# Kernel tuning notes

Measured on AMD Instinct MI355X. Metric: run time of the kernel, lower is better.

The kernel has to match this reference:

```python
import jax, jax.numpy as jnp
import numpy as np

B, S, HID = 2, 2048, 1024
H, D = 16, 64
R = 128  # max_relative_position
NREL = 2 * R + 1


def _make_indices():
    i = np.arange(S)[:, None]
    j = np.arange(S)[None, :]
    return np.clip(j - i + R, 0, 2 * R).astype(np.int32)  # [S, S]


def setup_inputs() -> dict:
    key = jax.random.key(0)
    ks = jax.random.split(key, 10)
    sc = 0.02
    return {
        "hidden_states": jax.random.normal(ks[0], (B, S, HID), jnp.float32),
        "st_mask": jnp.ones((B, S), jnp.float32),
        "Wq": jax.random.normal(ks[1], (HID, HID), jnp.float32) * sc,
        "bq": jnp.zeros((HID,), jnp.float32),
        "Wk": jax.random.normal(ks[2], (HID, HID), jnp.float32) * sc,
        "bk": jnp.zeros((HID,), jnp.float32),
        "Wv": jax.random.normal(ks[3], (HID, HID), jnp.float32) * sc,
        "bv": jnp.zeros((HID,), jnp.float32),
        "rel_key_emb": jax.random.normal(ks[4], (NREL, D), jnp.float32) * sc,
        "rel_val_emb": jax.random.normal(ks[5], (NREL, D), jnp.float32) * sc,
        "indices": jnp.asarray(_make_indices()),
    }


def reference(hidden_states, st_mask, Wq, bq, Wk, bk, Wv, bv, rel_key_emb, rel_val_emb, indices):
    b, s, _ = hidden_states.shape

    def heads(x):  # [B,S,HID] -> [B,H,S,D]
        return x.reshape(b, s, H, D).transpose(0, 2, 1, 3)

    q = heads(hidden_states @ Wq.T + bq)
    k = heads(hidden_states @ Wk.T + bk)
    v = heads(hidden_states @ Wv.T + bv)

    scores = jnp.einsum("bhqd,bhkd->bhqk", q, k) / jnp.sqrt(jnp.asarray(D, q.dtype))

    # relative position key bias: gather per (query, key) pair
    rel_scores = jnp.einsum("bhqd,rd->bhqr", q, rel_key_emb)  # [B,H,S,NREL]
    idx = indices[None, None]  # [1,1,S,S]
    scores = scores + jnp.take_along_axis(rel_scores, jnp.broadcast_to(idx, scores.shape), axis=3)

    mask = (1.0 - st_mask) * -10000.0  # [B,S]
    scores = scores + mask[:, None, None, :]

    probs = jax.nn.softmax(scores, axis=-1)  # dropout is identity at eval
    context = jnp.einsum("bhqk,bhkd->bhqd", probs, v)

    # scatter-add probs back onto relative buckets for the value path
    qi = jnp.arange(s)[:, None]  # [S,1] broadcasts with indices [S,S]
    rel_probs = jnp.zeros((b, H, s, NREL), probs.dtype).at[:, :, qi, indices].add(probs)
    context = context + jnp.einsum("bhqr,rd->bhqd", rel_probs, rel_val_emb)

    return context.transpose(0, 2, 1, 3).reshape(b, s, H * D)
```

## Files before the change

kernel.cpp:

```cpp
#include <hip/hip_runtime.h>
#include <math.h>

typedef __bf16 bf16;
typedef __bf16 bf16x8 __attribute__((ext_vector_type(8)));
typedef __bf16 bf16x4 __attribute__((ext_vector_type(4)));
typedef float  f32x4  __attribute__((ext_vector_type(4)));

namespace {
constexpr int B_ = 2, S_ = 2048, HID_ = 1024, H_ = 16, D_ = 64, R_ = 128, NREL_ = 257;
constexpr float LOG2E_ = 1.44269504f;
constexpr float QSC_ = 0.125f * LOG2E_;
}

static __device__ __forceinline__ f32x4 mfma16(bf16x8 a, bf16x8 b, f32x4 c) {
  return __builtin_amdgcn_mfma_f32_16x16x32_bf16(a, b, c, 0, 0, 0);
}
static __device__ __forceinline__ void split2(float f, bf16 &hi, bf16 &lo) {
  hi = (bf16)f; lo = (bf16)(f - (float)hi);
}
static __device__ __forceinline__ void gload16(const bf16* g, bf16* l) {
  __builtin_amdgcn_global_load_lds(
      (const __attribute__((address_space(1))) void*)g,
      (__attribute__((address_space(3))) void*)l, 16, 0, 0);
}

__global__ __launch_bounds__(256) void prep_kernel(
    const float* __restrict__ st_mask, const float* __restrict__ rkE,
    const float* __restrict__ rvE, const float* __restrict__ hidden,
    const float* __restrict__ Wq, const float* __restrict__ Wk,
    const float* __restrict__ Wv,
    float* __restrict__ msk2, bf16* __restrict__ rkEb, bf16* __restrict__ rvTb,
    bf16* __restrict__ Ahg, bf16* __restrict__ Alg, bf16* __restrict__ Wbg)
{
  const int t0 = blockIdx.x * 256 + threadIdx.x;
  const int NT = gridDim.x * 256;
  for (int t = t0; t < B_ * S_; t += NT)
    msk2[t] = (1.f - st_mask[t]) * -10000.f * LOG2E_;
  for (int t = t0; t < 272 * 64; t += NT) {
    const int bk = t >> 6, d = t & 63;
    rkEb[t] = (bk < NREL_) ? (bf16)(rkE[bk * D_ + d] * 8.0f) : (bf16)0.f;
  }
  for (int t = t0; t < 64 * 288; t += NT) {
    const int d = t / 288, c = t - d * 288;
    rvTb[t] = (c < NREL_) ? (bf16)rvE[c * D_ + d] : (bf16)0.f;
  }
  for (int t = t0; t < (B_ * S_ * HID_) / 4; t += NT) {
    const float4 a = ((const float4*)hidden)[t];
    const float av[4] = {a.x, a.y, a.z, a.w};
    bf16x4 h, o;
#pragma unroll
    for (int i = 0; i < 4; ++i) {
      bf16 th, tl;
      split2(av[i], th, tl);
      h[i] = th; o[i] = tl;
    }
    *(bf16x4*)&Ahg[t * 4] = h;
    *(bf16x4*)&Alg[t * 4] = o;
  }
  for (int t = t0; t < 3 * (HID_ * HID_) / 4; t += NT) {
    const int s = t >> 18, i = t & 262143;
    const float4 wv4 = ((const float4*)(s == 0 ? Wq : s == 1 ? Wk : Wv))[i];
    bf16x4 h;
    h[0] = (bf16)wv4.x; h[1] = (bf16)wv4.y; h[2] = (bf16)wv4.z; h[3] = (bf16)wv4.w;
    *(bf16x4*)&Wbg[s * 1048576 + i * 4] = h;
  }
}

__global__ __launch_bounds__(256, 2) void qkv_mfma_kernel(
    const bf16* __restrict__ Ahg, const bf16* __restrict__ Alg,
    const bf16* __restrict__ Wbg,
    const float* __restrict__ bq, const float* __restrict__ bk,
    const float* __restrict__ bv,
    bf16* __restrict__ Qh, bf16* __restrict__ Ql,
    bf16* __restrict__ Kb, bf16* __restrict__ Vt)
{
  const int swz = ((int)blockIdx.x & 7) * 64 + ((int)blockIdx.x >> 3);
  const int m0 = (swz >> 4) * 128;
  const int n0 = (swz & 15) * 64;
  const int tid = threadIdx.x;
  const int l = tid & 63, w = tid >> 6;
  const int cl = l & 15, g = l >> 4;

  __shared__ __align__(16) bf16 AhS[2][4096];
  __shared__ __align__(16) bf16 AlS[2][4096];
  __shared__ __align__(16) bf16 WS[2][3][2048];

  const int r0 = tid >> 2;
  const int csw = (((tid & 3) ^ (r0 & 3)) << 3);
  const size_t aoff0 = (size_t)(m0 + r0) * HID_ + csw;
  const size_t aoff1 = (size_t)(m0 + 64 + r0) * HID_ + csw;
  const size_t woff  = (size_t)(n0 + r0) * HID_ + csw;
  const int wb = w * 512;

  const int rA0 = w * 16 + cl;
  const int eA0 = rA0 * 32 + 8 * (g ^ (rA0 & 3));
  const int eA1 = eA0 + 2048;
  const int eW  = cl * 32 + 8 * (g ^ (cl & 3));

  f32x4 acc[2][3][4];
#pragma unroll
  for (int hf = 0; hf < 2; ++hf)
#pragma unroll
    for (int s = 0; s < 3; ++s)
#pragma unroll
      for (int nf = 0; nf < 4; ++nf)
#pragma unroll
        for (int i = 0; i < 4; ++i) acc[hf][s][nf][i] = 0.f;

  gload16(Ahg + aoff0, &AhS[0][wb]);
  gload16(Ahg + aoff1, &AhS[0][2048 + wb]);
  gload16(Alg + aoff0, &AlS[0][wb]);
  gload16(Alg + aoff1, &AlS[0][2048 + wb]);
  gload16(Wbg + woff,           &WS[0][0][wb]);
  gload16(Wbg + 1048576 + woff, &WS[0][1][wb]);
  gload16(Wbg + 2097152 + woff, &WS[0][2][wb]);
  __syncthreads();

  int cur = 0;
  for (int kt = 0; kt < HID_ / 32; ++kt) {
    if (kt + 1 < HID_ / 32) {
      const size_t ko = (size_t)(kt + 1) * 32;
      bf16* ah = &AhS[cur ^ 1][0]; bf16* al = &AlS[cur ^ 1][0];
      gload16(Ahg + aoff0 + ko, ah + wb);
      gload16(Ahg + aoff1 + ko, ah + 2048 + wb);
      gload16(Alg + aoff0 + ko, al + wb);
      gload16(Alg + aoff1 + ko, al + 2048 + wb);
      gload16(Wbg + woff + ko,           &WS[cur ^ 1][0][wb]);
      gload16(Wbg + 1048576 + woff + ko, &WS[cur ^ 1][1][wb]);
      gload16(Wbg + 2097152 + woff + ko, &WS[cur ^ 1][2][wb]);
    }

    const bf16x8 fah0 = *(const bf16x8*)&AhS[cur][eA0];
    const bf16x8 fah1 = *(const bf16x8*)&AhS[cur][eA1];
    const bf16x8 fal0 = *(const bf16x8*)&AlS[cur][eA0];
    const bf16x8 fal1 = *(const bf16x8*)&AlS[cur][eA1];
#pragma unroll
    for (int s = 0; s < 3; ++s)
#pragma unroll
      for (int nf = 0; nf < 4; ++nf) {
        const bf16x8 fb = *(const bf16x8*)&WS[cur][s][nf * 512 + eW];
        acc[0][s][nf] = mfma16(fah0, fb, acc[0][s][nf]);
        acc[0][s][nf] = mfma16(fal0, fb, acc[0][s][nf]);
        acc[1][s][nf] = mfma16(fah1, fb, acc[1][s][nf]);
        acc[1][s][nf] = mfma16(fal1, fb, acc[1][s][nf]);
      }
    __syncthreads();
    cur ^= 1;
  }

  const float* bs_[3] = {bq, bk, bv};
#pragma unroll
  for (int s = 0; s < 3; ++s)
#pragma unroll
    for (int nf = 0; nf < 4; ++nf) {
      const int n = n0 + nf * 16 + cl;
      const float bias = bs_[s][n];
      const int hd = n >> 6, d = n & 63;
#pragma unroll
      for (int hf = 0; hf < 2; ++hf)
#pragma unroll
        for (int reg = 0; reg < 4; ++reg) {
          const int m = m0 + hf * 64 + w * 16 + g * 4 + reg;
          const int b = m >> 11, sq = m & (S_ - 1);
          const float val = acc[hf][s][nf][reg] + bias;
          if (s == 0) {
            bf16 h, o; split2(val * QSC_, h, o);
            const size_t idx = ((size_t)(b * H_ + hd) * S_ + sq) * D_ + d;
            Qh[idx] = h; Ql[idx] = o;
          } else if (s == 1) {
            Kb[((size_t)(b * H_ + hd) * S_ + sq) * D_ + d] = (bf16)val;
          } else {
            Vt[(((size_t)(b * H_ + hd) * (S_ / 32) + (sq >> 5)) * D_ + d) * 32 + (sq & 31)]
                = (bf16)val;
          }
        }
    }
}

__global__ __launch_bounds__(512, 4) void attn_kernel(
    const bf16* __restrict__ Qh, const bf16* __restrict__ Ql,
    const bf16* __restrict__ Kb, const bf16* __restrict__ Vt,
    const float* __restrict__ msk2, const bf16* __restrict__ rkEb,
    const bf16* __restrict__ rvTb, float* __restrict__ out)
{
  const int swz = ((int)blockIdx.x & 7) * 128 + ((int)blockIdx.x >> 3);
  const int qt = swz & 31, h = (swz >> 5) & 15, b = swz >> 9;
  const int q0 = qt * 64;
  const int tid = threadIdx.x;
  const int l = tid & 63, w = tid >> 6;
  const int wq = (w & 3) * 16;
  const int wh = w >> 2;
  const int cl = l & 15, g = l >> 4, kg8 = g * 8;
  const int lq = wq + cl;

  __shared__ __align__(16) bf16 k_s[2][4096];
  __shared__ __align__(16) bf16 v_s[2][4096];
  __shared__ __align__(16) bf16 T[64][288];
  __shared__ __align__(16) bf16 ph[64][72];
  __shared__ float red[2][3][64];
  __shared__ float lsum_s[64];

  const size_t bh = (size_t)(b * H_ + h) * S_;
  const bf16* Kbase = Kb + bh * D_;
  const bf16* Vbase = Vt + bh * D_;
  const float* mbase = msk2 + b * S_;

  const int tKr = tid >> 3;
  const int koff = tKr * 64 + (((tid & 7) ^ (tKr & 7)) << 3);
  const int tVs = tid >> 8, tVu = tid & 255, tVd = tVu >> 2;
  const int voff = tVs * 2048 + tVd * 32 + ((((tVu & 3) ^ (tVd & 3))) << 3);
  bf16* kdst0 = &k_s[0][w * 512]; bf16* kdst1 = &k_s[1][w * 512];
  bf16* vdst0 = &v_s[0][w * 512]; bf16* vdst1 = &v_s[1][w * 512];

  gload16(Kbase + koff, kdst0);
  gload16(Vbase + voff, vdst0);

  bf16x8 qh0, qh1, ql0, ql1;
  {
    const size_t base = (bh + q0 + lq) * D_ + kg8;
    qh0 = *(const bf16x8*)(Qh + base);
    qh1 = *(const bf16x8*)(Qh + base + 32);
    ql0 = *(const bf16x8*)(Ql + base);
    ql1 = *(const bf16x8*)(Ql + base + 32);
  }

  {
    const int nt0 = wh ? 9 : 0, ntE = wh ? 17 : 9;
    for (int nt = nt0; nt < ntE; ++nt) {
      f32x4 r; r[0] = r[1] = r[2] = r[3] = 0.f;
      const bf16x8 a0 = *(const bf16x8*)(rkEb + (size_t)(nt * 16 + cl) * 64 + kg8);
      const bf16x8 a1 = *(const bf16x8*)(rkEb + (size_t)(nt * 16 + cl) * 64 + 32 + kg8);
      r = mfma16(a0, qh0, r); r = mfma16(a0, ql0, r);
      r = mfma16(a1, qh1, r); r = mfma16(a1, ql1, r);
      bf16x4 pk;
#pragma unroll
      for (int reg = 0; reg < 4; ++reg) pk[reg] = (bf16)r[reg];
      *(bf16x4*)&T[lq][nt * 16 + g * 4] = pk;
    }
  }
  __syncthreads();

  const float rs_lo = (float)T[lq][0];
  const float rs_hi = (float)T[lq][2 * R_];
  const int qg = q0 + lq;

  f32x4 ctx0, ctx1;
#pragma unroll
  for (int i = 0; i < 4; ++i) { ctx0[i] = 0.f; ctx1[i] = 0.f; }
  float lsum = 0.f, plo = 0.f, phi = 0.f;

  const int r00 = wh * 32 + cl, r10 = wh * 32 + 16 + cl;
  const int ksw = (r00 & 7);
  const int rd0 = wh * 32 + cl, rd1 = wh * 32 + 16 + cl;
  const int vsw = (rd0 & 3);
  const int e00 = r00 * 64 + 8 * (g ^ ksw),  e01 = r00 * 64 + 8 * ((4 + g) ^ ksw);
  const int e10 = r10 * 64 + 8 * (g ^ ksw),  e11 = r10 * 64 + 8 * ((4 + g) ^ ksw);
  const int f0 = rd0 * 32 + 8 * (g ^ vsw),   f1 = rd1 * 32 + 8 * (g ^ vsw);

  int cur = 0;
  for (int kt = 0; kt < S_ / 64; ++kt) {
    if (kt + 1 < S_ / 64) {
      gload16(Kbase + (size_t)(kt + 1) * 4096 + koff, cur ? kdst0 : kdst1);
      gload16(Vbase + (size_t)(kt + 1) * 4096 + voff, cur ? vdst0 : vdst1);
    }

    const bf16* kc = &k_s[cur][0];
    const bf16x8 a00 = *(const bf16x8*)&kc[e00];
    const bf16x8 a01 = *(const bf16x8*)&kc[e01];
    const bf16x8 a10 = *(const bf16x8*)&kc[e10];
    const bf16x8 a11 = *(const bf16x8*)&kc[e11];

    f32x4 s0, s1;
    s0[0]=s0[1]=s0[2]=s0[3]=0.f; s1[0]=s1[1]=s1[2]=s1[3]=0.f;
    s0 = mfma16(a00, qh0, s0); s0 = mfma16(a00, ql0, s0);
    s0 = mfma16(a01, qh1, s0); s0 = mfma16(a01, ql1, s0);
    s1 = mfma16(a10, qh0, s1); s1 = mfma16(a10, ql0, s1);
    s1 = mfma16(a11, qh1, s1); s1 = mfma16(a11, ql1, s1);

    const int j0 = kt * 64 + wh * 32;
    const float4 mk0 = *(const float4*)(mbase + j0 + g * 4);
    const float4 mk1 = *(const float4*)(mbase + j0 + 16 + g * 4);
    const int dlt = kt * 64 - q0;
    const int mode = (dlt <= -192) ? 0 : (dlt >= 192 ? 1 : 2);

#pragma unroll
    for (int nf = 0; nf < 2; ++nf) {
      const f32x4 sa = nf ? s1 : s0;
      const float4 mkv = nf ? mk1 : mk0;
      const float mks[4] = {mkv.x, mkv.y, mkv.z, mkv.w};
      float p[4];
      if (mode == 0) {
#pragma unroll
        for (int reg = 0; reg < 4; ++reg) p[reg] = exp2f(sa[reg] + rs_lo + mks[reg]);
        plo += (p[0] + p[1]) + (p[2] + p[3]);
      } else if (mode == 1) {
#pragma unroll
        for (int reg = 0; reg < 4; ++reg) p[reg] = exp2f(sa[reg] + rs_hi + mks[reg]);
        phi += (p[0] + p[1]) + (p[2] + p[3]);
      } else {
        const int jb = j0 + nf * 16 + g * 4;
#pragma unroll
        for (int reg = 0; reg < 4; ++reg) {
          const int bkv = jb + reg - qg + R_;
          const int bkc = bkv < 0 ? 0 : (bkv > 2 * R_ ? 2 * R_ : bkv);
          const float pv = exp2f(sa[reg] + (float)T[lq][bkc] + mks[reg]);
          p[reg] = pv;
          if (bkv <= 0)           plo += pv;
          else if (bkv >= 2 * R_) phi += pv;
          else                    T[lq][bkv] = (bf16)pv;
        }
      }
      lsum += (p[0] + p[1]) + (p[2] + p[3]);
      bf16x4 pk;
#pragma unroll
      for (int reg = 0; reg < 4; ++reg) pk[reg] = (bf16)p[reg];
      *(bf16x4*)&ph[lq][wh * 32 + nf * 16 + g * 4] = pk;
    }
    __syncthreads();

    const bf16x8 pa0 = *(const bf16x8*)&ph[lq][kg8];
    const bf16x8 pa1 = *(const bf16x8*)&ph[lq][32 + kg8];
    const bf16* vc = &v_s[cur][0];
    const bf16x8 vb00 = *(const bf16x8*)&vc[f0];
    const bf16x8 vb01 = *(const bf16x8*)&vc[2048 + f0];
    const bf16x8 vb10 = *(const bf16x8*)&vc[f1];
    const bf16x8 vb11 = *(const bf16x8*)&vc[2048 + f1];
    ctx0 = mfma16(pa0, vb00, ctx0); ctx0 = mfma16(pa1, vb01, ctx0);
    ctx1 = mfma16(pa0, vb10, ctx1); ctx1 = mfma16(pa1, vb11, ctx1);
    __syncthreads();
    cur ^= 1;
  }

  lsum += __shfl_xor(lsum, 16); lsum += __shfl_xor(lsum, 32);
  plo  += __shfl_xor(plo, 16);  plo  += __shfl_xor(plo, 32);
  phi  += __shfl_xor(phi, 16);  phi  += __shfl_xor(phi, 32);
  if (l < 16) {
    red[wh][0][wq + l] = lsum;
    red[wh][1][wq + l] = plo;
    red[wh][2][wq + l] = phi;
  }
  __syncthreads();
  if (tid < 64) {
    lsum_s[tid]    = red[0][0][tid] + red[1][0][tid];
    T[tid][0]      = (bf16)(red[0][1][tid] + red[1][1][tid]);
    T[tid][2 * R_] = (bf16)(red[0][2][tid] + red[1][2][tid]);
  }
  for (int t = tid; t < 64 * 32; t += 512) {
    const int c = t & 31;
    if (c) T[t >> 5][256 + c] = (bf16)0.f;
  }
  if (q0 < R_ || q0 > S_ - R_ - 64) {
    for (int t = tid; t < 64 * 256; t += 512) {
      const int r = t >> 8, c = t & 255;
      if (c >= 1) {
        const int j = q0 + r + c - R_;
        if (j < 0 || j >= S_) T[r][c] = (bf16)0.f;
      }
    }
  }
  __syncthreads();

#pragma unroll
  for (int ks = 0; ks < 9; ++ks) {
    const bf16x8 pa = *(const bf16x8*)&T[lq][ks * 32 + kg8];
    const bf16x8 v0 = *(const bf16x8*)(rvTb + (size_t)(wh * 32 + cl) * 288 + ks * 32 + kg8);
    const bf16x8 v1 = *(const bf16x8*)(rvTb + (size_t)(wh * 32 + 16 + cl) * 288 + ks * 32 + kg8);
    ctx0 = mfma16(pa, v0, ctx0);
    ctx1 = mfma16(pa, v1, ctx1);
  }

#pragma unroll
  for (int reg = 0; reg < 4; ++reg) {
    const int qrow = wq + g * 4 + reg;
    const float invl = 1.f / lsum_s[qrow];
    float* op = out + (size_t)(b * S_ + q0 + qrow) * HID_ + h * 64 + wh * 32;
    op[cl]      = ctx0[reg] * invl;
    op[16 + cl] = ctx1[reg] * invl;
  }
}

extern "C" void kernel_launch(void* const* d_in, const int* in_sizes, int n_in,
                              void* d_out, int out_size, void* d_ws, size_t ws_size,
                              hipStream_t stream)
{
  (void)in_sizes; (void)n_in; (void)out_size; (void)ws_size;
  const float* hidden  = (const float*)d_in[0];
  const float* st_mask = (const float*)d_in[1];
  const float* Wq = (const float*)d_in[2];
  const float* bq = (const float*)d_in[3];
  const float* Wk = (const float*)d_in[4];
  const float* bk = (const float*)d_in[5];
  const float* Wv = (const float*)d_in[6];
  const float* bv = (const float*)d_in[7];
  const float* rkE = (const float*)d_in[8];
  const float* rvE = (const float*)d_in[9];
  float* out = (float*)d_out;

  const size_t per = (size_t)B_ * H_ * S_ * D_;
  bf16* Qh   = (bf16*)d_ws;
  bf16* Ql   = Qh + per;
  bf16* Kb   = Ql + per;
  bf16* Vt   = Kb + per;
  bf16* Ahg  = Vt + per;
  bf16* Alg  = Ahg + per;
  bf16* Wbg  = Alg + per;
  bf16* rkEb = Wbg + 3 * 1048576;
  bf16* rvTb = rkEb + 272 * 64;
  float* msk2 = (float*)(rvTb + 64 * 288);

  prep_kernel<<<dim3(1024), 256, 0, stream>>>(
      st_mask, rkE, rvE, hidden, Wq, Wk, Wv, msk2, rkEb, rvTb, Ahg, Alg, Wbg);
  qkv_mfma_kernel<<<dim3(512), 256, 0, stream>>>(
      Ahg, Alg, Wbg, bq, bk, bv, Qh, Ql, Kb, Vt);
  attn_kernel<<<dim3(1024), 512, 0, stream>>>(
      Qh, Ql, Kb, Vt, msk2, rkEb, rvTb, out);
}
```

Baseline: 189.8 us.

## Move relative-bucket table to global scratch, retile V layout, add MFMA priority

The per-block relative-score/probability table T leaves LDS and goes to a global workspace region that reuses the dead Ahg buffer. This cuts LDS per block so more blocks fit per CU, and the launch bounds rise from 4 to 6 waves-per-EU to match. V is now stored in 64-row tiles so it can use the same swizzled load offsets as K, and s_setprio brackets the MFMA groups. The cost is that the gather and scatter into T in the diagonal band become global memory accesses with higher latency, which may offset the occupancy gain.

```diff
diff --git a/kernel.cpp b/kernel.cpp
--- a/kernel.cpp
+++ b/kernel.cpp
@@ -170,18 +170,19 @@
           } else if (s == 1) {
             Kb[((size_t)(b * H_ + hd) * S_ + sq) * D_ + d] = (bf16)val;
           } else {
-            Vt[(((size_t)(b * H_ + hd) * (S_ / 32) + (sq >> 5)) * D_ + d) * 32 + (sq & 31)]
+            Vt[(((size_t)(b * H_ + hd) * (S_ / 64) + (sq >> 6)) * D_ + d) * 64 + (sq & 63)]
                 = (bf16)val;
           }
         }
     }
 }
 
-__global__ __launch_bounds__(512, 4) void attn_kernel(
+__global__ __launch_bounds__(512, 6) void attn_kernel(
     const bf16* __restrict__ Qh, const bf16* __restrict__ Ql,
     const bf16* __restrict__ Kb, const bf16* __restrict__ Vt,
     const float* __restrict__ msk2, const bf16* __restrict__ rkEb,
-    const bf16* __restrict__ rvTb, float* __restrict__ out)
+    const bf16* __restrict__ rvTb, bf16* __restrict__ Tg,
+    float* __restrict__ out)
 {
   const int swz = ((int)blockIdx.x & 7) * 128 + ((int)blockIdx.x >> 3);
   const int qt = swz & 31, h = (swz >> 5) & 15, b = swz >> 9;
@@ -195,10 +196,12 @@
 
   __shared__ __align__(16) bf16 k_s[2][4096];
   __shared__ __align__(16) bf16 v_s[2][4096];
-  __shared__ __align__(16) bf16 T[64][288];
   __shared__ __align__(16) bf16 ph[64][72];
   __shared__ float red[2][3][64];
   __shared__ float lsum_s[64];
+
+  bf16* Tw = Tg + (size_t)swz * (64 * 288);
+  bf16* Tq = Tw + (size_t)lq * 288;
 
   const size_t bh = (size_t)(b * H_ + h) * S_;
   const bf16* Kbase = Kb + bh * D_;
@@ -207,8 +210,7 @@
 
   const int tKr = tid >> 3;
   const int koff = tKr * 64 + (((tid & 7) ^ (tKr & 7)) << 3);
-  const int tVs = tid >> 8, tVu = tid & 255, tVd = tVu >> 2;
-  const int voff = tVs * 2048 + tVd * 32 + ((((tVu & 3) ^ (tVd & 3))) << 3);
+  const int voff = koff;
   bf16* kdst0 = &k_s[0][w * 512]; bf16* kdst1 = &k_s[1][w * 512];
   bf16* vdst0 = &v_s[0][w * 512]; bf16* vdst1 = &v_s[1][w * 512];
 
@@ -235,13 +237,13 @@
       bf16x4 pk;
 #pragma unroll
       for (int reg = 0; reg < 4; ++reg) pk[reg] = (bf16)r[reg];
-      *(bf16x4*)&T[lq][nt * 16 + g * 4] = pk;
+      *(bf16x4*)&Tq[nt * 16 + g * 4] = pk;
     }
   }
   __syncthreads();
 
-  const float rs_lo = (float)T[lq][0];
-  const float rs_hi = (float)T[lq][2 * R_];
+  const float rs_lo = (float)Tq[0];
+  const float rs_hi = (float)Tq[2 * R_];
   const int qg = q0 + lq;
 
   f32x4 ctx0, ctx1;
@@ -250,12 +252,10 @@
   float lsum = 0.f, plo = 0.f, phi = 0.f;
 
   const int r00 = wh * 32 + cl, r10 = wh * 32 + 16 + cl;
-  const int ksw = (r00 & 7);
-  const int rd0 = wh * 32 + cl, rd1 = wh * 32 + 16 + cl;
-  const int vsw = (rd0 & 3);
-  const int e00 = r00 * 64 + 8 * (g ^ ksw),  e01 = r00 * 64 + 8 * ((4 + g) ^ ksw);
-  const int e10 = r10 * 64 + 8 * (g ^ ksw),  e11 = r10 * 64 + 8 * ((4 + g) ^ ksw);
-  const int f0 = rd0 * 32 + 8 * (g ^ vsw),   f1 = rd1 * 32 + 8 * (g ^ vsw);
+  const int e00 = r00 * 64 + 8 * (g ^ (r00 & 7)), e01 = r00 * 64 + 8 * ((4 + g) ^ (r00 & 7));
+  const int e10 = r10 * 64 + 8 * (g ^ (r10 & 7)), e11 = r10 * 64 + 8 * ((4 + g) ^ (r10 & 7));
+  const int f0  = r00 * 64 + 8 * (g ^ (r00 & 7)), f0b = r00 * 64 + 8 * ((4 + g) ^ (r00 & 7));
+  const int f1  = r10 * 64 + 8 * (g ^ (r10 & 7)), f1b = r10 * 64 + 8 * ((4 + g) ^ (r10 & 7));
 
   int cur = 0;
   for (int kt = 0; kt < S_ / 64; ++kt) {
@@ -272,10 +272,12 @@
 
     f32x4 s0, s1;
     s0[0]=s0[1]=s0[2]=s0[3]=0.f; s1[0]=s1[1]=s1[2]=s1[3]=0.f;
+    __builtin_amdgcn_s_setprio(1);
     s0 = mfma16(a00, qh0, s0); s0 = mfma16(a00, ql0, s0);
     s0 = mfma16(a01, qh1, s0); s0 = mfma16(a01, ql1, s0);
     s1 = mfma16(a10, qh0, s1); s1 = mfma16(a10, ql0, s1);
     s1 = mfma16(a11, qh1, s1); s1 = mfma16(a11, ql1, s1);
+    __builtin_amdgcn_s_setprio(0);
 
     const int j0 = kt * 64 + wh * 32;
     const float4 mk0 = *(const float4*)(mbase + j0 + g * 4);
@@ -303,11 +305,11 @@
         for (int reg = 0; reg < 4; ++reg) {
           const int bkv = jb + reg - qg + R_;
           const int bkc = bkv < 0 ? 0 : (bkv > 2 * R_ ? 2 * R_ : bkv);
-          const float pv = exp2f(sa[reg] + (float)T[lq][bkc] + mks[reg]);
+          const float pv = exp2f(sa[reg] + (float)Tq[bkc] + mks[reg]);
           p[reg] = pv;
           if (bkv <= 0)           plo += pv;
           else if (bkv >= 2 * R_) phi += pv;
-          else                    T[lq][bkv] = (bf16)pv;
+          else                    Tq[bkv] = (bf16)pv;
         }
       }
       lsum += (p[0] + p[1]) + (p[2] + p[3]);
@@ -322,11 +324,13 @@
     const bf16x8 pa1 = *(const bf16x8*)&ph[lq][32 + kg8];
     const bf16* vc = &v_s[cur][0];
     const bf16x8 vb00 = *(const bf16x8*)&vc[f0];
-    const bf16x8 vb01 = *(const bf16x8*)&vc[2048 + f0];
+    const bf16x8 vb01 = *(const bf16x8*)&vc[f0b];
     const bf16x8 vb10 = *(const bf16x8*)&vc[f1];
-    const bf16x8 vb11 = *(const bf16x8*)&vc[2048 + f1];
+    const bf16x8 vb11 = *(const bf16x8*)&vc[f1b];
+    __builtin_amdgcn_s_setprio(1);
     ctx0 = mfma16(pa0, vb00, ctx0); ctx0 = mfma16(pa1, vb01, ctx0);
     ctx1 = mfma16(pa0, vb10, ctx1); ctx1 = mfma16(pa1, vb11, ctx1);
+    __builtin_amdgcn_s_setprio(0);
     __syncthreads();
     cur ^= 1;
   }
@@ -341,20 +345,20 @@
   }
   __syncthreads();
   if (tid < 64) {
-    lsum_s[tid]    = red[0][0][tid] + red[1][0][tid];
-    T[tid][0]      = (bf16)(red[0][1][tid] + red[1][1][tid]);
-    T[tid][2 * R_] = (bf16)(red[0][2][tid] + red[1][2][tid]);
+    lsum_s[tid] = red[0][0][tid] + red[1][0][tid];
+    Tw[(size_t)tid * 288]          = (bf16)(red[0][1][tid] + red[1][1][tid]);
+    Tw[(size_t)tid * 288 + 2 * R_] = (bf16)(red[0][2][tid] + red[1][2][tid]);
   }
   for (int t = tid; t < 64 * 32; t += 512) {
     const int c = t & 31;
-    if (c) T[t >> 5][256 + c] = (bf16)0.f;
+    if (c) Tw[(size_t)(t >> 5) * 288 + 256 + c] = (bf16)0.f;
   }
   if (q0 < R_ || q0 > S_ - R_ - 64) {
     for (int t = tid; t < 64 * 256; t += 512) {
       const int r = t >> 8, c = t & 255;
       if (c >= 1) {
         const int j = q0 + r + c - R_;
-        if (j < 0 || j >= S_) T[r][c] = (bf16)0.f;
+        if (j < 0 || j >= S_) Tw[(size_t)r * 288 + c] = (bf16)0.f;
       }
     }
   }
@@ -362,11 +366,13 @@
 
 #pragma unroll
   for (int ks = 0; ks < 9; ++ks) {
-    const bf16x8 pa = *(const bf16x8*)&T[lq][ks * 32 + kg8];
+    const bf16x8 pa = *(const bf16x8*)&Tq[ks * 32 + kg8];
     const bf16x8 v0 = *(const bf16x8*)(rvTb + (size_t)(wh * 32 + cl) * 288 + ks * 32 + kg8);
     const bf16x8 v1 = *(const bf16x8*)(rvTb + (size_t)(wh * 32 + 16 + cl) * 288 + ks * 32 + kg8);
+    __builtin_amdgcn_s_setprio(1);
     ctx0 = mfma16(pa, v0, ctx0);
     ctx1 = mfma16(pa, v1, ctx1);
+    __builtin_amdgcn_s_setprio(0);
   }
 
 #pragma unroll
@@ -397,21 +403,24 @@
   float* out = (float*)d_out;
 
   const size_t per = (size_t)B_ * H_ * S_ * D_;
-  bf16* Qh   = (bf16*)d_ws;
-  bf16* Ql   = Qh + per;
-  bf16* Kb   = Ql + per;
-  bf16* Vt   = Kb + per;
-  bf16* Ahg  = Vt + per;
-  bf16* Alg  = Ahg + per;
-  bf16* Wbg  = Alg + per;
-  bf16* rkEb = Wbg + 3 * 1048576;
-  bf16* rvTb = rkEb + 272 * 64;
-  float* msk2 = (float*)(rvTb + 64 * 288);
+  char* wsb = (char*)d_ws;
+  float* msk2 = (float*)wsb;
+  bf16*  rkEb = (bf16*)(wsb + 16384);
+  bf16*  rvTb = (bf16*)(wsb + 16384 + 34816);
+  char*  base1 = wsb + 16384 + 34816 + 36864;
+  bf16* Qh = (bf16*)base1;
+  bf16* Ql = Qh + per;
+  bf16* Kb = Ql + per;
+  bf16* Vt = Kb + per;
+  bf16* Ahg = Vt + per;
+  bf16* Alg = Ahg + per;
+  bf16* Wbg = Alg + per;
+  bf16* Tg  = Ahg;
 
   prep_kernel<<<dim3(1024), 256, 0, stream>>>(
       st_mask, rkE, rvE, hidden, Wq, Wk, Wv, msk2, rkEb, rvTb, Ahg, Alg, Wbg);
   qkv_mfma_kernel<<<dim3(512), 256, 0, stream>>>(
       Ahg, Alg, Wbg, bq, bk, bv, Qh, Ql, Kb, Vt);
   attn_kernel<<<dim3(1024), 512, 0, stream>>>(
-      Qh, Ql, Kb, Vt, msk2, rkEb, rvTb, out);
-}
+      Qh, Ql, Kb, Vt, msk2, rkEb, rvTb, Tg, out);
+}
```

Result: slower. 228.3 us (+20.3%).
